# Performance work log

Measured on AMD Instinct MI355X. Metric: run time of the kernel, lower is better.

## Reference

```python
import jax, jax.numpy as jnp
import numpy as np
import math

ALPHA = 0.6
BETA = 0.4
NPTS = 1000   # trapezoid points, matches beta_cdf default npts
EPS = 1e-10   # lower integration limit, matches zeros(...) + 1e-10
# log Beta(alpha, beta) normalizer
BETALN = math.lgamma(ALPHA) + math.lgamma(BETA) - math.lgamma(ALPHA + BETA)


def beta_logpdf(x):
    # torch.distributions.Beta(ALPHA, BETA).log_prob(x)
    return (ALPHA - 1.0) * jnp.log(x) + (BETA - 1.0) * jnp.log1p(-x) - BETALN


def setup_inputs() -> dict:
    key = jax.random.key(0)
    # probabilities in (0,1); uniform like a sigmoid-gate output
    x = jax.random.uniform(key, (512, 128), dtype=jnp.float32)
    return {"x": x}


def reference(x):
    n, c = x.shape
    sorted_x = jnp.sort(x, axis=0)                                  # [n, c]
    # linspace grid from EPS to each sorted value: [NPTS, n, c]
    steps = (jnp.arange(NPTS, dtype=x.dtype) / (NPTS - 1))[:, None, None]
    grid = EPS + steps * (sorted_x - EPS)
    pdf = jnp.exp(beta_logpdf(grid))                                # [NPTS, n, c]
    # replicate torch's check: skip first point if pdf(EPS) > 1
    # (static: depends only on the fixed alpha/beta constants)
    pdf0 = math.exp((ALPHA - 1.0) * math.log(EPS)
                    + (BETA - 1.0) * math.log1p(-EPS) - BETALN)
    start = 1 if pdf0 > 1.0 else 0
    g = grid[start:]
    p = pdf[start:]
    # trapezoidal rule along the integration axis -> pcdf [n, c]
    pcdf = 0.5 * jnp.sum((p[1:] + p[:-1]) * (g[1:] - g[:-1]), axis=0)
    ecdf = (jnp.arange(1, n + 1, dtype=x.dtype) / (n + 1))[:, None]  # [n, 1]
    # sum of squared CDF gaps over all columns, divided by n
    loss = jnp.sum((pcdf - ecdf) ** 2) / n
    return loss
```

## Files before the change

### kernel.cpp

```cpp
#include <hip/hip_runtime.h>
#include <cmath>

#define N_ROWS 512
#define N_COLS 128

__device__ __forceinline__ float betacf_c(const float a, const float b, float x) {
    const float qab = a + b, qap = a + 1.0f, qam = a - 1.0f;
    float c = 1.0f;
    float d = fmaf(-(qab / qap), x, 1.0f);
    if (fabsf(d) < 1e-30f) d = 1e-30f;
    d = __fdividef(1.0f, d);
    float h = d;
    #pragma unroll
    for (int m = 1; m <= 16; ++m) {
        const float fm = (float)m, m2 = 2.0f * fm;
        const float c1 = fm * (b - fm) / ((qam + m2) * (a + m2));
        float aa = c1 * x;
        d = fmaf(aa, d, 1.0f); if (fabsf(d) < 1e-30f) d = 1e-30f;
        c = 1.0f + __fdividef(aa, c); if (fabsf(c) < 1e-30f) c = 1e-30f;
        d = __fdividef(1.0f, d);
        h *= d * c;
        const float c2 = -(a + fm) * (qab + fm) / ((a + m2) * (qap + m2));
        aa = c2 * x;
        d = fmaf(aa, d, 1.0f); if (fabsf(d) < 1e-30f) d = 1e-30f;
        c = 1.0f + __fdividef(aa, c); if (fabsf(c) < 1e-30f) c = 1e-30f;
        d = __fdividef(1.0f, d);
        h *= d * c;
    }
    return h;
}

__global__ __launch_bounds__(256) void rank_loss(const float* __restrict__ x,
                                                 float* __restrict__ out,
                                                 float lnB, float invB, float c_head) {
    __shared__ __align__(16) float colv[N_ROWS];
    const int tid  = threadIdx.x;
    const int col  = blockIdx.x >> 1;
    const int half = blockIdx.x & 1;
    colv[tid]       = x[tid * N_COLS + col];
    colv[tid + 256] = x[(tid + 256) * N_COLS + col];
    __syncthreads();

    const int   myidx = half * 256 + tid;
    const float mine  = colv[myidx];

    int rank = 0;
    #pragma unroll 4
    for (int j4 = 0; j4 < N_ROWS / 4; ++j4) {
        const float4 o = *reinterpret_cast<const float4*>(&colv[j4 * 4]);
        const int jb = j4 * 4;
        rank += (int)(o.x < mine || (o.x == mine && (jb + 0) < myidx));
        rank += (int)(o.y < mine || (o.y == mine && (jb + 1) < myidx));
        rank += (int)(o.z < mine || (o.z == mine && (jb + 2) < myidx));
        rank += (int)(o.w < mine || (o.w == mine && (jb + 3) < myidx));
    }

    const float s  = fmaxf(mine, 1e-30f);
    const float sm = s - 1e-10f;
    const float h  = sm * (1.0f / 999.0f);
    const float x1 = 1e-10f + h;

    const float ls  = __logf(s);
    const float om  = fmaxf(1.0f - s, 1e-30f);
    const float lom = __logf(om);
    const float bt  = __expf(fmaf(0.6f, ls, fmaf(0.4f, lom, -lnB)));
    float I;
    if (s < 0.53333333f)
        I = bt * betacf_c(0.6f, 0.4f, s) * (1.0f / 0.6f);
    else
        I = 1.0f - bt * betacf_c(0.4f, 0.6f, om) * (1.0f / 0.4f);

    const float head = c_head * __expf(0.6f * __logf(x1));

    const float sm04 = __expf(-0.4f * ls);
    float wp_m06 = __expf(-0.6f * lom);
    float wp_p04 = om * wp_m06;
    float dr = 0.0f;
    #pragma unroll
    for (int j = 1; j <= 8; ++j) {
        float w    = fmaf((float)j, h, om);
        float wm06 = __expf(-0.6f * __logf(w));
        float wp04 = w * wm06;
        dr += 0.5f * h * (wp_m06 + wm06) - (wp04 - wp_p04) * 2.5f;
        wp_m06 = wm06; wp_p04 = wp04;
    }
    dr *= sm04 * invB;

    const float T    = I - head + dr;
    const float ecdf = (float)(rank + 1) * (1.0f / 513.0f);
    const float d    = T - ecdf;
    float val = d * d;

    #pragma unroll
    for (int off = 32; off > 0; off >>= 1)
        val += __shfl_down(val, off);
    __shared__ float wsum[4];
    if ((tid & 63) == 0) wsum[tid >> 6] = val;
    __syncthreads();
    if (tid == 0)
        atomicAdd(out, (wsum[0] + wsum[1] + wsum[2] + wsum[3]) * (1.0f / (float)N_ROWS));
}

extern "C" void kernel_launch(void* const* d_in, const int* in_sizes, int n_in,
                              void* d_out, int out_size, void* d_ws, size_t ws_size,
                              hipStream_t stream) {
    const float* x = (const float*)d_in[0];
    float* out = (float*)d_out;

    const double B = exp(lgamma(0.6) + lgamma(0.4) - lgamma(1.0));
    const float lnB    = (float)log(B);
    const float invB   = (float)(1.0 / B);
    const float c_head = (float)(1.0 / (0.6 * B) - 0.03185 / B);

    rank_loss<<<2 * N_COLS, 256, 0, stream>>>(x, out, lnB, invB, c_head);
}
```

Before: 73.26 us.

## Split rank counting across four lanes per element and reduce partials in second kernel

Each element's rank count over its column is now split across four threads, each scanning a quarter of the column with staggered offsets to reduce LDS bank conflicts, then combined with xor shuffles. The grid grows from 256 to 1024 blocks (8 segments per column), raising parallelism and shortening each thread's serial loop. The final sum now goes through a per-block partials buffer and a separate single-block reduce kernel instead of atomics. In exchange, the beta CDF math is computed redundantly by four lanes, the column is loaded four times more overall, and there is an extra kernel launch.

```diff
diff --git a/kernel.cpp b/kernel.cpp
--- a/kernel.cpp
+++ b/kernel.cpp
@@ -3,6 +3,7 @@
 
 #define N_ROWS 512
 #define N_COLS 128
+#define RL_BLOCKS (N_COLS * 8)
 
 __device__ __forceinline__ float betacf_c(const float a, const float b, float x) {
     const float qab = a + b, qap = a + 1.0f, qam = a - 1.0f;
@@ -31,29 +32,33 @@
 }
 
 __global__ __launch_bounds__(256) void rank_loss(const float* __restrict__ x,
-                                                 float* __restrict__ out,
+                                                 float* __restrict__ partials,
                                                  float lnB, float invB, float c_head) {
     __shared__ __align__(16) float colv[N_ROWS];
-    const int tid  = threadIdx.x;
-    const int col  = blockIdx.x >> 1;
-    const int half = blockIdx.x & 1;
+    const int tid = threadIdx.x;
+    const int col = blockIdx.x >> 3;
+    const int seg = blockIdx.x & 7;
     colv[tid]       = x[tid * N_COLS + col];
     colv[tid + 256] = x[(tid + 256) * N_COLS + col];
     __syncthreads();
 
-    const int   myidx = half * 256 + tid;
+    const int   q     = tid & 3;
+    const int   myidx = seg * 64 + (tid >> 2);
     const float mine  = colv[myidx];
 
     int rank = 0;
-    #pragma unroll 4
-    for (int j4 = 0; j4 < N_ROWS / 4; ++j4) {
-        const float4 o = *reinterpret_cast<const float4*>(&colv[j4 * 4]);
-        const int jb = j4 * 4;
+    #pragma unroll
+    for (int i = 0; i < 32; ++i) {
+        const int c4 = (i + 2 * q) & 31;
+        const int jb = q * 128 + c4 * 4;
+        const float4 o = *reinterpret_cast<const float4*>(&colv[jb]);
         rank += (int)(o.x < mine || (o.x == mine && (jb + 0) < myidx));
         rank += (int)(o.y < mine || (o.y == mine && (jb + 1) < myidx));
         rank += (int)(o.z < mine || (o.z == mine && (jb + 2) < myidx));
         rank += (int)(o.w < mine || (o.w == mine && (jb + 3) < myidx));
     }
+    rank += __shfl_xor(rank, 1);
+    rank += __shfl_xor(rank, 2);
 
     const float s  = fmaxf(mine, 1e-30f);
     const float sm = s - 1e-10f;
@@ -88,8 +93,8 @@
 
     const float T    = I - head + dr;
     const float ecdf = (float)(rank + 1) * (1.0f / 513.0f);
-    const float d    = T - ecdf;
-    float val = d * d;
+    const float dd   = T - ecdf;
+    float val = (q == 0) ? dd * dd : 0.0f;
 
     #pragma unroll
     for (int off = 32; off > 0; off >>= 1)
@@ -98,7 +103,25 @@
     if ((tid & 63) == 0) wsum[tid >> 6] = val;
     __syncthreads();
     if (tid == 0)
-        atomicAdd(out, (wsum[0] + wsum[1] + wsum[2] + wsum[3]) * (1.0f / (float)N_ROWS));
+        partials[blockIdx.x] = wsum[0] + wsum[1] + wsum[2] + wsum[3];
+}
+
+__global__ __launch_bounds__(256) void reduce_partials(const float* __restrict__ partials,
+                                                       float* __restrict__ out) {
+    float acc = 0.0f;
+    #pragma unroll
+    for (int k = 0; k < RL_BLOCKS / 256; ++k)
+        acc += partials[threadIdx.x + k * 256];
+    #pragma unroll
+    for (int off = 32; off > 0; off >>= 1)
+        acc += __shfl_down(acc, off);
+    __shared__ float w[4];
+    const int lane = threadIdx.x & 63;
+    const int wv   = threadIdx.x >> 6;
+    if (lane == 0) w[wv] = acc;
+    __syncthreads();
+    if (threadIdx.x == 0)
+        out[0] = (w[0] + w[1] + w[2] + w[3]) * (1.0f / (float)N_ROWS);
 }
 
 extern "C" void kernel_launch(void* const* d_in, const int* in_sizes, int n_in,
@@ -106,11 +129,13 @@
                               hipStream_t stream) {
     const float* x = (const float*)d_in[0];
     float* out = (float*)d_out;
+    float* partials = (float*)d_ws;
 
     const double B = exp(lgamma(0.6) + lgamma(0.4) - lgamma(1.0));
     const float lnB    = (float)log(B);
     const float invB   = (float)(1.0 / B);
     const float c_head = (float)(1.0 / (0.6 * B) - 0.03185 / B);
 
-    rank_loss<<<2 * N_COLS, 256, 0, stream>>>(x, out, lnB, invB, c_head);
+    rank_loss<<<RL_BLOCKS, 256, 0, stream>>>(x, partials, lnB, invB, c_head);
+    reduce_partials<<<1, 256, 0, stream>>>(partials, out);
 }
```

Measured after the change: 71.71 us. -2.1%, faster.
